# Kernel tuning notes

Hardware: AMD Instinct MI355X
Metric: run time of the kernel (lower is better)

The kernel has to match this reference:

```python
import jax, jax.numpy as jnp
import numpy as np

N = 80         # max_num_nodes
ITERS = 50     # mpm max_iters


def setup_inputs() -> dict:
    key = jax.random.key(0)
    k1, k2 = jax.random.split(key)
    # reconstructed (predicted) adjacency probabilities, kept strictly in (0,1) for BCE
    recon = jax.random.uniform(k1, (N, N), jnp.float32) * 0.98 + 0.01
    # ground-truth binary adjacency, symmetric with self-loops (adj[i,i] used in S build)
    adj = (jax.random.uniform(k2, (N, N), jnp.float32) > 0.5).astype(jnp.float32)
    adj = jnp.maximum(adj, adj.T)
    adj = adj.at[jnp.arange(N), jnp.arange(N)].set(1.0)
    return {"recon_grf": recon, "original_grf": adj}


def _forward(recon, adj):
    # degree-like matching features
    out_features = jnp.sum(recon, axis=1)   # recon node features g_a
    adj_features = jnp.sum(adj, axis=1)     # original node features f_i

    adj_d = jnp.diagonal(adj)               # adj[i,i]
    rec_d = jnp.diagonal(recon)             # recon[a,a]
    eye = jnp.eye(N, dtype=recon.dtype)
    off = 1.0 - eye

    # off-diagonal edge affinities (zero when i==j or a==b, matching the loop skips)
    src = adj * adj_d[:, None] * adj_d[None, :] * off     # [i,j] = adj[i,j]*adj[i,i]*adj[j,j]
    tgt = recon * rec_d[:, None] * rec_d[None, :] * off   # [a,b] = recon[a,b]*recon[a,a]*recon[b,b]

    # diagonal affinities S[i,i,a,a] = adj[i,i]*recon[a,a]*sim(f_i, g_a)
    sim = 1.0 / (jnp.abs(adj_features[:, None] - out_features[None, :]) + 1.0)  # [i,a]
    d = adj_d[:, None] * rec_d[None, :] * sim                                   # [i,a]

    # full affinity tensor S[i,j,a,b]  (N^4 elements)
    S = src[:, :, None, None] * tgt[None, None, :, :] \
        + (eye[:, :, None, None] * eye[None, None, :, :]) * d[:, None, :, None]

    # max-pooling matching (mpm), 50 iterations; checkpoint keeps vjp memory at 1 iter
    @jax.checkpoint
    def step(x):
        # pooled[i,j,a] = max_b x[j,b] * S[i,j,a,b]
        pooled = jnp.max(x[None, :, None, :] * S, axis=3)     # [i,j,a]
        neigh = jnp.sum(pooled * off[:, :, None], axis=1)     # sum over j != i -> [i,a]
        x_new = x * d + neigh                                 # d[i,a] == S[i,i,a,a]
        return x_new / jnp.linalg.norm(x_new)

    x0 = jnp.full((N, N), 1.0 / N, dtype=recon.dtype)
    assignment, _ = jax.lax.scan(lambda x, _: (step(x), None), x0, None, length=ITERS)

    # BCE on the upper triangle (incl. diagonal), mean reduction like F.binary_cross_entropy
    iu = jnp.triu_indices(N)
    t = adj[iu]
    p = recon[iu]
    loss = -jnp.mean(t * jnp.log(p) + (1.0 - t) * jnp.log(1.0 - p))
    return loss, assignment


def reference(recon_grf, original_grf):
    return _forward(recon_grf, original_grf)
```

## Files before the change

kernel.cpp:

```cpp
#include <hip/hip_runtime.h>
#include <math.h>

#define NN 80
#define MITERS 50
#define NTHREADS 1024

typedef _Float16 h8 __attribute__((ext_vector_type(8)));
typedef float f4 __attribute__((ext_vector_type(4)));

__device__ __forceinline__ unsigned pk_mul_f16(unsigned a, unsigned b) {
  unsigned d; asm("v_pk_mul_f16 %0, %1, %2" : "=v"(d) : "v"(a), "v"(b)); return d;
}
__device__ __forceinline__ unsigned pk_max_f16(unsigned a, unsigned b) {
  unsigned d; asm("v_pk_max_f16 %0, %1, %2" : "=v"(d) : "v"(a), "v"(b)); return d;
}
__device__ __forceinline__ h8 as_h8(uint4 u) {
  union { uint4 u; h8 h; } x; x.u = u; return x.h;
}

#define OFF_XH    0
#define OFF_TT    13120
#define OFF_MM    26240
#define OFF_SRCH  59520
#define OFF_DLT   76160
#define OFF_FR    103040
#define OFF_FA    103360
#define OFF_RD    103680
#define OFF_AD    104000
#define OFF_WSUM  104320
#define OFF_LSUM  104448
#define LDS_BYTES 104512

#define PB(r, k) ((((r) >> 2) * 656) + (((k) >> 1) * 16) + (((r) & 3) * 4) + (((k) & 1) * 2))


#define DO_TILE(I0, A0, XO)                                                   \
  {                                                                           \
    f4 acc = {0.f, 0.f, 0.f, 0.f};                                            \
    _Pragma("unroll")                                                         \
    for (int ks = 0; ks < 3; ++ks) {                                          \
      const uint4 afr =                                                       \
          *(const uint4*)(SRCHb + ((I0) + la) * 208 + ks * 64 + gr * 16);     \
      const int blk = (ks * 4 + gr) ^ mkey;                                   \
      const int mo = ((A0) + la) * 208 + blk * 16;                            \
      const uint4 b0 = *(const uint4*)(MMb + mo);                             \
      const uint4 b1 = *(const uint4*)(MMb + 16640 + mo);                     \
      uint4 bb;                                                               \
      bb.x = pk_max_f16(b0.x, b1.x);                                          \
      bb.y = pk_max_f16(b0.y, b1.y);                                          \
      bb.z = pk_max_f16(b0.z, b1.z);                                          \
      bb.w = pk_max_f16(b0.w, b1.w);                                          \
      acc = __builtin_amdgcn_mfma_f32_16x16x32_f16(as_h8(afr),                \
                                                   as_h8(bb), acc, 0, 0, 0);  \
    }                                                                         \
    const int col = (A0) + la;                                                \
    const int rb = (I0) + gr * 4;                                             \
    const float4 dl = *(const float4*)(DLTb + col * 336 + rb * 4);            \
    const float n0 = fmaf(XO[0], dl.x, acc[0]) * inv;                         \
    const float n1 = fmaf(XO[1], dl.y, acc[1]) * inv;                         \
    const float n2 = fmaf(XO[2], dl.z, acc[2]) * inv;                         \
    const float n3 = fmaf(XO[3], dl.w, acc[3]) * inv;                         \
    ss += n0 * n0 + n1 * n1 + n2 * n2 + n3 * n3;                              \
    XO[0] = n0; XO[1] = n1; XO[2] = n2; XO[3] = n3;                           \
    char* xa = XHb + (((I0) >> 2) + gr) * 656 + (col >> 1) * 16 + (col & 1) * 2; \
    *(_Float16*)(xa) = (_Float16)n0;                                          \
    *(_Float16*)(xa + 4) = (_Float16)n1;                                      \
    *(_Float16*)(xa + 8) = (_Float16)n2;                                      \
    *(_Float16*)(xa + 12) = (_Float16)n3;                                     \
  }

__global__ void __launch_bounds__(NTHREADS, 4)
grf_kernel(const float* __restrict__ recon, const float* __restrict__ adj,
           float* __restrict__ out) {
  extern __shared__ char ldsb[];
  char* XHb = ldsb + OFF_XH;
  char* TTb = ldsb + OFF_TT;
  char* MMb = ldsb + OFF_MM;
  char* SRCHb = ldsb + OFF_SRCH;
  char* DLTb = ldsb + OFF_DLT;
  float* FR = (float*)(ldsb + OFF_FR);
  float* FA = (float*)(ldsb + OFF_FA);
  float* RD = (float*)(ldsb + OFF_RD);
  float* AD = (float*)(ldsb + OFF_AD);
  float* WSUM = (float*)(ldsb + OFF_WSUM);
  float* LSUM = (float*)(ldsb + OFF_LSUM);

  const int t = threadIdx.x;
  const int wave = t >> 6, lane = t & 63;
  const int la = lane & 15, gr = lane >> 4;
  const int mkey = (la >> 2) & 3;

  if (t < 80) {
    float s = 0.f;
    for (int b = 0; b < NN; ++b) s += recon[t * NN + b];
    FR[t] = s;
    RD[t] = recon[t * NN + t];
  } else if (t < 160) {
    const int i = t - 80;
    float s = 0.f;
    for (int j = 0; j < NN; ++j) s += adj[i * NN + j];
    FA[i] = s;
    AD[i] = adj[i * NN + i];
  }
  if (t < 32) {
    const float q = (float)(_Float16)(1.0f / 80.0f);
    WSUM[t] = (t == 0) ? 6400.0f * q * q : 0.f;
  }
  __syncthreads();

  float lacc = 0.f;
  for (int f = t; f < NN * NN; f += NTHREADS) {
    const int r = f / NN, c = f - (f / NN) * NN;
    *(_Float16*)(XHb + PB(r, c)) = (_Float16)(1.0f / 80.0f);
    const float tv = (r == c) ? 0.f : recon[r * NN + c] * RD[r] * RD[c];
    *(_Float16*)(TTb + PB(r, c)) = (_Float16)tv;
    *(float*)(DLTb + (c * 84 + r) * 4) =
        AD[r] * RD[c] / (fabsf(FA[r] - FR[c]) + 1.f);
    const float sv = (r == c) ? 0.f : adj[r * NN + c] * AD[r] * AD[c];
    *(_Float16*)(SRCHb + (r * 104 + c) * 2) = (_Float16)sv;
    if (c >= r) {
      const float tb = adj[f], p = recon[f];
      lacc -= tb * logf(p) + (1.f - tb) * logf(1.f - p);
    }
  }
  for (int f = t; f < 1920; f += NTHREADS) {
    const int r = f / 24, j = 80 + (f - (f / 24) * 24);
    *(_Float16*)(SRCHb + (r * 104 + j) * 2) = (_Float16)0.f;
  }
  for (int f = t; f < 8320; f += NTHREADS) *(unsigned*)(MMb + f * 4) = 0u;

  #pragma unroll
  for (int off = 32; off > 0; off >>= 1) lacc += __shfl_down(lacc, off, 64);
  if (lane == 0) LSUM[wave] = lacc;
  __syncthreads();
  if (t == 0) {
    float s = 0.f;
    for (int w = 0; w < 16; ++w) s += LSUM[w];
    out[0] = s / 3240.f;
  }

  const int i00 = (wave / 5) * 16, a00 = (wave % 5) * 16;
  const int tt1 = wave + 16;
  const bool has2 = tt1 < 25;
  const int i01 = has2 ? (tt1 / 5) * 16 : 0;
  const int a01 = has2 ? (tt1 % 5) * 16 : 0;

  const int g = t >> 9;
  const int u = t & 511;
  const bool actA = (u < 400);
  const int rt = u / 20;
  const int ct = u - rt * 20;
  const char* xAp = XHb + rt * 656 + g * 320;
  const char* tAp = TTb + ct * 656 + g * 320;
  char* mwp = MMb + g * 16640 + (ct * 4) * 208 +
              (((rt >> 1) ^ (ct & 3)) * 16) + ((rt & 1) * 8);

  float xo0[4], xo1[4];
  #pragma unroll
  for (int k = 0; k < 4; ++k) xo0[k] = xo1[k] = (float)(_Float16)(1.0f / 80.0f);

  for (int it = 0; it < MITERS; ++it) {
    if (actA) {
      unsigned m[4][4];
      #pragma unroll
      for (int r = 0; r < 4; ++r)
        #pragma unroll
        for (int c = 0; c < 4; ++c) m[r][c] = 0u;
      #pragma unroll 4
      for (int cc = 0; cc < 20; ++cc) {
        const uint4 xq = *(const uint4*)(xAp + cc * 16);
        const uint4 tq = *(const uint4*)(tAp + cc * 16);
        const unsigned xr[4] = {xq.x, xq.y, xq.z, xq.w};
        const unsigned tc[4] = {tq.x, tq.y, tq.z, tq.w};
        #pragma unroll
        for (int r = 0; r < 4; ++r)
          #pragma unroll
          for (int c = 0; c < 4; ++c)
            m[r][c] = pk_max_f16(m[r][c], pk_mul_f16(xr[r], tc[c]));
      }
      #pragma unroll
      for (int c = 0; c < 4; ++c) {
        unsigned lo[4];
        #pragma unroll
        for (int r = 0; r < 4; ++r) {
          const unsigned v = m[r][c];
          lo[r] = pk_max_f16(v, (v >> 16) | (v << 16)) & 0xffffu;
        }
        const uint2 w = make_uint2(lo[0] | (lo[1] << 16), lo[2] | (lo[3] << 16));
        *(uint2*)(mwp + c * 208) = w;
      }
    }
    __syncthreads();

    const float* WIN = WSUM + ((it & 1) << 4);
    const float4 wa = *(const float4*)(WIN);
    const float4 wb = *(const float4*)(WIN + 4);
    const float4 wc = *(const float4*)(WIN + 8);
    const float4 wd = *(const float4*)(WIN + 12);
    const float tot = ((wa.x + wa.y) + (wa.z + wa.w)) +
                      ((wb.x + wb.y) + (wb.z + wb.w)) +
                      ((wc.x + wc.y) + (wc.z + wc.w)) +
                      ((wd.x + wd.y) + (wd.z + wd.w));
    const float inv = 1.0f / sqrtf(tot);

    float ss = 0.f;
    DO_TILE(i00, a00, xo0);
    if (has2) DO_TILE(i01, a01, xo1);

    #pragma unroll
    for (int off = 32; off > 0; off >>= 1) ss += __shfl_down(ss, off, 64);
    if (lane == 0) WSUM[(((it + 1) & 1) << 4) + wave] = ss;
    __syncthreads();
  }

  {
    const float* WF = WSUM + ((MITERS & 1) << 4);
    float tot = 0.f;
    #pragma unroll
    for (int w = 0; w < 16; ++w) tot += WF[w];
    const float finv = 1.0f / sqrtf(tot);
    for (int f = t; f < NN * NN; f += NTHREADS) {
      const int i = f / NN, a = f - (f / NN) * NN;
      out[1 + f] = (float)*(const _Float16*)(XHb + PB(i, a)) * finv;
    }
  }
}

extern "C" void kernel_launch(void* const* d_in, const int* in_sizes, int n_in,
                              void* d_out, int out_size, void* d_ws, size_t ws_size,
                              hipStream_t stream) {
  const float* recon = (const float*)d_in[0];
  const float* adj   = (const float*)d_in[1];
  float* out = (float*)d_out;
  (void)in_sizes; (void)n_in; (void)out_size; (void)d_ws; (void)ws_size;

  hipFuncSetAttribute(reinterpret_cast<const void*>(grf_kernel),
                      hipFuncAttributeMaxDynamicSharedMemorySize, LDS_BYTES);
  grf_kernel<<<1, NTHREADS, LDS_BYTES, stream>>>(recon, adj, out);
}
```

Baseline: 368.4 us.

## Switch X/T to row-major swizzled LDS layouts, transpose MFMA operands, DPP reductions

The assignment matrix X moves from a packed 4-row block layout to plain row-major with padding, and T to row-major with an XOR swizzle. The max-pool inner loop is rewritten to load four X rows and one T row per chunk. MFMA operands are swapped so each lane writes four contiguous halves as one packed 8-byte store. The wave sum-of-squares reduction now uses DPP instead of shuffles, and one idle thread precomputes the norm total so other threads read a single value. The intent is fewer LDS instructions and bank conflicts and less reduction latency on the serial 50-iteration path. The risk is new bank conflicts or higher register pressure in the reworked loop.

```diff
diff --git a/kernel.cpp b/kernel.cpp
--- a/kernel.cpp
+++ b/kernel.cpp
@@ -6,6 +6,7 @@
 #define NTHREADS 1024
 
 typedef _Float16 h8 __attribute__((ext_vector_type(8)));
+typedef _Float16 h2 __attribute__((ext_vector_type(2)));
 typedef float f4 __attribute__((ext_vector_type(4)));
 
 __device__ __forceinline__ unsigned pk_mul_f16(unsigned a, unsigned b) {
@@ -17,32 +18,33 @@
 __device__ __forceinline__ h8 as_h8(uint4 u) {
   union { uint4 u; h8 h; } x; x.u = u; return x.h;
 }
+template <int CTRL>
+__device__ __forceinline__ float dpp_add(float x) {
+  int yi = __builtin_amdgcn_update_dpp(0, __builtin_bit_cast(int, x),
+                                       CTRL, 0xf, 0xf, true);
+  return x + __builtin_bit_cast(float, yi);
+}
 
 #define OFF_XH    0
-#define OFF_TT    13120
-#define OFF_MM    26240
-#define OFF_SRCH  59520
-#define OFF_DLT   76160
-#define OFF_FR    103040
-#define OFF_FA    103360
-#define OFF_RD    103680
-#define OFF_AD    104000
-#define OFF_WSUM  104320
-#define OFF_LSUM  104448
-#define LDS_BYTES 104512
-
-#define PB(r, k) ((((r) >> 2) * 656) + (((k) >> 1) * 16) + (((r) & 3) * 4) + (((k) & 1) * 2))
-
+#define OFF_TT    14080
+#define OFF_MM    29440
+#define OFF_SRCH  62720
+#define OFF_DL    79360
+#define OFF_FR    106240
+#define OFF_FA    106560
+#define OFF_RD    106880
+#define OFF_AD    107200
+#define OFF_WSUM  107520
+#define OFF_TOT   107648
+#define OFF_LSUM  107664
+#define LDS_BYTES 107728
 
 #define DO_TILE(I0, A0, XO)                                                   \
   {                                                                           \
     f4 acc = {0.f, 0.f, 0.f, 0.f};                                            \
     _Pragma("unroll")                                                         \
     for (int ks = 0; ks < 3; ++ks) {                                          \
-      const uint4 afr =                                                       \
-          *(const uint4*)(SRCHb + ((I0) + la) * 208 + ks * 64 + gr * 16);     \
-      const int blk = (ks * 4 + gr) ^ mkey;                                   \
-      const int mo = ((A0) + la) * 208 + blk * 16;                            \
+      const int mo = ((A0) + la) * 208 + (((ks * 4 + gr) ^ mkey) * 16);       \
       const uint4 b0 = *(const uint4*)(MMb + mo);                             \
       const uint4 b1 = *(const uint4*)(MMb + 16640 + mo);                     \
       uint4 bb;                                                               \
@@ -50,23 +52,25 @@
       bb.y = pk_max_f16(b0.y, b1.y);                                          \
       bb.z = pk_max_f16(b0.z, b1.z);                                          \
       bb.w = pk_max_f16(b0.w, b1.w);                                          \
-      acc = __builtin_amdgcn_mfma_f32_16x16x32_f16(as_h8(afr),                \
-                                                   as_h8(bb), acc, 0, 0, 0);  \
+      const uint4 afr =                                                       \
+          *(const uint4*)(SRCHb + ((I0) + la) * 208 + ks * 64 + gr * 16);     \
+      acc = __builtin_amdgcn_mfma_f32_16x16x32_f16(as_h8(bb),                 \
+                                                   as_h8(afr), acc, 0, 0, 0); \
     }                                                                         \
-    const int col = (A0) + la;                                                \
-    const int rb = (I0) + gr * 4;                                             \
-    const float4 dl = *(const float4*)(DLTb + col * 336 + rb * 4);            \
+    const int iN = (I0) + la;                                                 \
+    const int ab = (A0) + gr * 4;                                             \
+    const float4 dl = *(const float4*)(DLb + iN * 336 + ab * 4);              \
     const float n0 = fmaf(XO[0], dl.x, acc[0]) * inv;                         \
     const float n1 = fmaf(XO[1], dl.y, acc[1]) * inv;                         \
     const float n2 = fmaf(XO[2], dl.z, acc[2]) * inv;                         \
     const float n3 = fmaf(XO[3], dl.w, acc[3]) * inv;                         \
     ss += n0 * n0 + n1 * n1 + n2 * n2 + n3 * n3;                              \
     XO[0] = n0; XO[1] = n1; XO[2] = n2; XO[3] = n3;                           \
-    char* xa = XHb + (((I0) >> 2) + gr) * 656 + (col >> 1) * 16 + (col & 1) * 2; \
-    *(_Float16*)(xa) = (_Float16)n0;                                          \
-    *(_Float16*)(xa + 4) = (_Float16)n1;                                      \
-    *(_Float16*)(xa + 8) = (_Float16)n2;                                      \
-    *(_Float16*)(xa + 12) = (_Float16)n3;                                     \
+    const unsigned ulo = __builtin_bit_cast(                                  \
+        unsigned, __builtin_amdgcn_cvt_pkrtz(n0, n1));                        \
+    const unsigned uhi = __builtin_bit_cast(                                  \
+        unsigned, __builtin_amdgcn_cvt_pkrtz(n2, n3));                        \
+    *(uint2*)(XHb + iN * 176 + ab * 2) = make_uint2(ulo, uhi);                \
   }
 
 __global__ void __launch_bounds__(NTHREADS, 4)
@@ -77,12 +81,13 @@
   char* TTb = ldsb + OFF_TT;
   char* MMb = ldsb + OFF_MM;
   char* SRCHb = ldsb + OFF_SRCH;
-  char* DLTb = ldsb + OFF_DLT;
+  char* DLb = ldsb + OFF_DL;
   float* FR = (float*)(ldsb + OFF_FR);
   float* FA = (float*)(ldsb + OFF_FA);
   float* RD = (float*)(ldsb + OFF_RD);
   float* AD = (float*)(ldsb + OFF_AD);
   float* WSUM = (float*)(ldsb + OFF_WSUM);
+  float* TOT = (float*)(ldsb + OFF_TOT);
   float* LSUM = (float*)(ldsb + OFF_LSUM);
 
   const int t = threadIdx.x;
@@ -104,20 +109,21 @@
   }
   if (t < 32) {
     const float q = (float)(_Float16)(1.0f / 80.0f);
-    WSUM[t] = (t == 0) ? 6400.0f * q * q : 0.f;
+    WSUM[t] = ((t & 15) == 0) ? 6400.0f * q * q : 0.f;
   }
   __syncthreads();
 
   float lacc = 0.f;
   for (int f = t; f < NN * NN; f += NTHREADS) {
     const int r = f / NN, c = f - (f / NN) * NN;
-    *(_Float16*)(XHb + PB(r, c)) = (_Float16)(1.0f / 80.0f);
+    *(_Float16*)(XHb + r * 176 + c * 2) = (_Float16)(1.0f / 80.0f);
     const float tv = (r == c) ? 0.f : recon[r * NN + c] * RD[r] * RD[c];
-    *(_Float16*)(TTb + PB(r, c)) = (_Float16)tv;
-    *(float*)(DLTb + (c * 84 + r) * 4) =
+    *(_Float16*)(TTb + r * 192 + (((c >> 3) ^ ((r >> 2) & 3)) * 16) +
+                 (c & 7) * 2) = (_Float16)tv;
+    *(float*)(DLb + (r * 84 + c) * 4) =
         AD[r] * RD[c] / (fabsf(FA[r] - FR[c]) + 1.f);
     const float sv = (r == c) ? 0.f : adj[r * NN + c] * AD[r] * AD[c];
-    *(_Float16*)(SRCHb + (r * 104 + c) * 2) = (_Float16)sv;
+    *(_Float16*)(SRCHb + r * 208 + c * 2) = (_Float16)sv;
     if (c >= r) {
       const float tb = adj[f], p = recon[f];
       lacc -= tb * logf(p) + (1.f - tb) * logf(1.f - p);
@@ -125,7 +131,7 @@
   }
   for (int f = t; f < 1920; f += NTHREADS) {
     const int r = f / 24, j = 80 + (f - (f / 24) * 24);
-    *(_Float16*)(SRCHb + (r * 104 + j) * 2) = (_Float16)0.f;
+    *(_Float16*)(SRCHb + r * 208 + j * 2) = (_Float16)0.f;
   }
   for (int f = t; f < 8320; f += NTHREADS) *(unsigned*)(MMb + f * 4) = 0u;
 
@@ -150,8 +156,9 @@
   const bool actA = (u < 400);
   const int rt = u / 20;
   const int ct = u - rt * 20;
-  const char* xAp = XHb + rt * 656 + g * 320;
-  const char* tAp = TTb + ct * 656 + g * 320;
+  const char* xrow = XHb + (rt * 4) * 176 + g * 80;
+  const char* trow = TTb + (ct * 4) * 192;
+  const int tkey = ct & 3;
   char* mwp = MMb + g * 16640 + (ct * 4) * 208 +
               (((rt >> 1) ^ (ct & 3)) * 16) + ((rt & 1) * 8);
 
@@ -166,17 +173,33 @@
       for (int r = 0; r < 4; ++r)
         #pragma unroll
         for (int c = 0; c < 4; ++c) m[r][c] = 0u;
-      #pragma unroll 4
-      for (int cc = 0; cc < 20; ++cc) {
-        const uint4 xq = *(const uint4*)(xAp + cc * 16);
-        const uint4 tq = *(const uint4*)(tAp + cc * 16);
-        const unsigned xr[4] = {xq.x, xq.y, xq.z, xq.w};
-        const unsigned tc[4] = {tq.x, tq.y, tq.z, tq.w};
+      #pragma unroll
+      for (int ch = 0; ch < 5; ++ch) {
+        const uint4 xq0 = *(const uint4*)(xrow + 0 * 176 + ch * 16);
+        const uint4 xq1 = *(const uint4*)(xrow + 1 * 176 + ch * 16);
+        const uint4 xq2 = *(const uint4*)(xrow + 2 * 176 + ch * 16);
+        const uint4 xq3 = *(const uint4*)(xrow + 3 * 176 + ch * 16);
+        const int tco = (((g * 5 + ch) ^ tkey) * 16);
         #pragma unroll
-        for (int r = 0; r < 4; ++r)
-          #pragma unroll
-          for (int c = 0; c < 4; ++c)
-            m[r][c] = pk_max_f16(m[r][c], pk_mul_f16(xr[r], tc[c]));
+        for (int c = 0; c < 4; ++c) {
+          const uint4 tq = *(const uint4*)(trow + c * 192 + tco);
+          m[0][c] = pk_max_f16(m[0][c], pk_mul_f16(xq0.x, tq.x));
+          m[0][c] = pk_max_f16(m[0][c], pk_mul_f16(xq0.y, tq.y));
+          m[0][c] = pk_max_f16(m[0][c], pk_mul_f16(xq0.z, tq.z));
+          m[0][c] = pk_max_f16(m[0][c], pk_mul_f16(xq0.w, tq.w));
+          m[1][c] = pk_max_f16(m[1][c], pk_mul_f16(xq1.x, tq.x));
+          m[1][c] = pk_max_f16(m[1][c], pk_mul_f16(xq1.y, tq.y));
+          m[1][c] = pk_max_f16(m[1][c], pk_mul_f16(xq1.z, tq.z));
+          m[1][c] = pk_max_f16(m[1][c], pk_mul_f16(xq1.w, tq.w));
+          m[2][c] = pk_max_f16(m[2][c], pk_mul_f16(xq2.x, tq.x));
+          m[2][c] = pk_max_f16(m[2][c], pk_mul_f16(xq2.y, tq.y));
+          m[2][c] = pk_max_f16(m[2][c], pk_mul_f16(xq2.z, tq.z));
+          m[2][c] = pk_max_f16(m[2][c], pk_mul_f16(xq2.w, tq.w));
+          m[3][c] = pk_max_f16(m[3][c], pk_mul_f16(xq3.x, tq.x));
+          m[3][c] = pk_max_f16(m[3][c], pk_mul_f16(xq3.y, tq.y));
+          m[3][c] = pk_max_f16(m[3][c], pk_mul_f16(xq3.z, tq.z));
+          m[3][c] = pk_max_f16(m[3][c], pk_mul_f16(xq3.w, tq.w));
+        }
       }
       #pragma unroll
       for (int c = 0; c < 4; ++c) {
@@ -186,30 +209,31 @@
           const unsigned v = m[r][c];
           lo[r] = pk_max_f16(v, (v >> 16) | (v << 16)) & 0xffffu;
         }
-        const uint2 w = make_uint2(lo[0] | (lo[1] << 16), lo[2] | (lo[3] << 16));
-        *(uint2*)(mwp + c * 208) = w;
+        *(uint2*)(mwp + c * 208) =
+            make_uint2(lo[0] | (lo[1] << 16), lo[2] | (lo[3] << 16));
       }
+    } else if (t == 1023) {
+      const float* W = WSUM + ((it & 1) << 4);
+      float s = 0.f;
+      #pragma unroll
+      for (int w = 0; w < 16; ++w) s += W[w];
+      TOT[it & 1] = s;
     }
     __syncthreads();
 
-    const float* WIN = WSUM + ((it & 1) << 4);
-    const float4 wa = *(const float4*)(WIN);
-    const float4 wb = *(const float4*)(WIN + 4);
-    const float4 wc = *(const float4*)(WIN + 8);
-    const float4 wd = *(const float4*)(WIN + 12);
-    const float tot = ((wa.x + wa.y) + (wa.z + wa.w)) +
-                      ((wb.x + wb.y) + (wb.z + wb.w)) +
-                      ((wc.x + wc.y) + (wc.z + wc.w)) +
-                      ((wd.x + wd.y) + (wd.z + wd.w));
-    const float inv = 1.0f / sqrtf(tot);
+    const float inv = 1.0f / sqrtf(TOT[it & 1]);
 
     float ss = 0.f;
     DO_TILE(i00, a00, xo0);
     if (has2) DO_TILE(i01, a01, xo1);
 
-    #pragma unroll
-    for (int off = 32; off > 0; off >>= 1) ss += __shfl_down(ss, off, 64);
-    if (lane == 0) WSUM[(((it + 1) & 1) << 4) + wave] = ss;
+    ss = dpp_add<0x111>(ss);
+    ss = dpp_add<0x112>(ss);
+    ss = dpp_add<0x114>(ss);
+    ss = dpp_add<0x118>(ss);
+    ss = dpp_add<0x142>(ss);
+    ss = dpp_add<0x143>(ss);
+    if (lane == 63) WSUM[(((it + 1) & 1) << 4) + wave] = ss;
     __syncthreads();
   }
 
@@ -221,7 +245,7 @@
     const float finv = 1.0f / sqrtf(tot);
     for (int f = t; f < NN * NN; f += NTHREADS) {
       const int i = f / NN, a = f - (f / NN) * NN;
-      out[1 + f] = (float)*(const _Float16*)(XHb + PB(i, a)) * finv;
+      out[1 + f] = (float)*(const _Float16*)(XHb + i * 176 + a * 2) * finv;
     }
   }
 }
@@ -234,7 +258,8 @@
   float* out = (float*)d_out;
   (void)in_sizes; (void)n_in; (void)out_size; (void)d_ws; (void)ws_size;
 
-  hipFuncSetAttribute(reinterpret_cast<const void*>(grf_kernel),
-                      hipFuncAttributeMaxDynamicSharedMemorySize, LDS_BYTES);
+  (void)hipFuncSetAttribute(reinterpret_cast<const void*>(grf_kernel),
+                            hipFuncAttributeMaxDynamicSharedMemorySize,
+                            LDS_BYTES);
   grf_kernel<<<1, NTHREADS, LDS_BYTES, stream>>>(recon, adj, out);
 }
```

New measurement: 350.6 us. 1.05x faster.
